# Performance work log

Measured on AMD Instinct MI355X. Metric: run time of the kernel, lower is better.

Reference implementation:

```python
import jax, jax.numpy as jnp
import numpy as np

N_NODES = 50000
N_EDGES = 1600000
IN_FEAT = 128
OUT_FEAT = 128


def setup_inputs() -> dict:
    key = jax.random.key(0)
    k_x, k_w, k_v, k_r, k_c = jax.random.split(key, 5)
    X = jax.random.normal(k_x, (N_NODES, IN_FEAT), dtype=jnp.float32)
    # nn.Linear(in_feat, out_feat, bias=False) weight: [out_feat, in_feat]
    W = jax.random.normal(k_w, (OUT_FEAT, IN_FEAT), dtype=jnp.float32) * (1.0 / np.sqrt(IN_FEAT))
    # Sparse adjacency A in COO form: A[rows[e], cols[e]] = vals[e]
    A_vals = jax.random.uniform(k_v, (N_EDGES,), dtype=jnp.float32)
    A_rows = jax.random.randint(k_r, (N_EDGES,), 0, N_NODES, dtype=jnp.int32)
    A_cols = jax.random.randint(k_c, (N_EDGES,), 0, N_NODES, dtype=jnp.int32)
    return {"X": X, "W": W, "A_vals": A_vals, "A_rows": A_rows, "A_cols": A_cols}


def reference(X, W, A_vals, A_rows, A_cols):
    # H = linear(X) = X @ W.T  -> [N, out_feat]
    H = jnp.einsum("ni,oi->no", X, W)
    # out = A @ H via COO SpMM: gather source rows, scale by edge value,
    # scatter-add into destination rows.
    msgs = A_vals[:, None] * H[A_cols]            # [E, out_feat]
    out = jax.ops.segment_sum(msgs, A_rows, num_segments=N_NODES)
    return out
```

## Files before the change

### kernel.cpp

```cpp
#include <hip/hip_runtime.h>


constexpr int N_NODES = 50000;
constexpr int N_EDGES = 1600000;
constexpr int FEAT    = 128;

constexpr int ROWS_PER_BIN = 64;
constexpr int NB           = (N_NODES + ROWS_PER_BIN - 1) / ROWS_PER_BIN;
constexpr int CAP          = 2560;
constexpr int CHUNK        = 4096;
constexpr int PART_BLOCKS  = (N_EDGES + CHUNK - 1) / CHUNK;
constexpr int GEMM_BLOCKS  = (N_NODES + 63) / 64;
constexpr int OVF_CAP      = 8192;

constexpr int SROWS = 16;
constexpr int SCAP  = 832;

__device__ __forceinline__ unsigned short f2bf(float x) {
    unsigned u = __float_as_uint(x);
    u += 0x7fffu + ((u >> 16) & 1u);
    return (unsigned short)(u >> 16);
}
__device__ __forceinline__ float bf2f(unsigned short s) {
    return __uint_as_float(((unsigned)s) << 16);
}

__global__ __launch_bounds__(256) void gemm_xwt_bf16(
    const float* __restrict__ X, const float* __restrict__ W,
    unsigned short* __restrict__ Hb, int* __restrict__ zbuf, int zn) {
    int zt = blockIdx.x * 256 + threadIdx.x;
    if (zt < zn) zbuf[zt] = 0;

    constexpr int BM = 64, BK = 32;
    __shared__ float Xs[BK][BM + 4];
    __shared__ float Ws[BK][FEAT + 4];

    const int tid = threadIdx.x;
    const int tx  = tid & 15;
    const int ty  = tid >> 4;
    const int row0 = blockIdx.x * BM;

    float acc[4][8];
#pragma unroll
    for (int i = 0; i < 4; i++)
#pragma unroll
        for (int j = 0; j < 8; j++) acc[i][j] = 0.f;

    for (int kt = 0; kt < FEAT; kt += BK) {
#pragma unroll
        for (int t = 0; t < 2; t++) {
            int idx = tid + 256 * t;
            int r   = idx >> 3;
            int kq  = (idx & 7) << 2;
            int gr  = row0 + r;
            if (gr >= N_NODES) gr = N_NODES - 1;
            const float4 v = *(const float4*)&X[gr * FEAT + kt + kq];
            Xs[kq + 0][r] = v.x; Xs[kq + 1][r] = v.y;
            Xs[kq + 2][r] = v.z; Xs[kq + 3][r] = v.w;
        }
#pragma unroll
        for (int t = 0; t < 4; t++) {
            int idx = tid + 256 * t;
            int o   = idx >> 3;
            int kq  = (idx & 7) << 2;
            const float4 v = *(const float4*)&W[o * FEAT + kt + kq];
            Ws[kq + 0][o] = v.x; Ws[kq + 1][o] = v.y;
            Ws[kq + 2][o] = v.z; Ws[kq + 3][o] = v.w;
        }
        __syncthreads();

#pragma unroll
        for (int k = 0; k < BK; k++) {
            const float4 xv = *(const float4*)&Xs[k][4 * ty];
            const float4 w0 = *(const float4*)&Ws[k][4 * tx];
            const float4 w1 = *(const float4*)&Ws[k][64 + 4 * tx];
            const float xa[4] = {xv.x, xv.y, xv.z, xv.w};
            const float wa[8] = {w0.x, w0.y, w0.z, w0.w, w1.x, w1.y, w1.z, w1.w};
#pragma unroll
            for (int i = 0; i < 4; i++)
#pragma unroll
                for (int j = 0; j < 8; j++) acc[i][j] += xa[i] * wa[j];
        }
        __syncthreads();
    }

    unsigned* Hb2 = (unsigned*)Hb;
#pragma unroll
    for (int i = 0; i < 4; i++) {
        int gr = row0 + 4 * ty + i;
        if (gr < N_NODES) {
            unsigned p0 = f2bf(acc[i][0]) | ((unsigned)f2bf(acc[i][1]) << 16);
            unsigned p1 = f2bf(acc[i][2]) | ((unsigned)f2bf(acc[i][3]) << 16);
            unsigned p2 = f2bf(acc[i][4]) | ((unsigned)f2bf(acc[i][5]) << 16);
            unsigned p3 = f2bf(acc[i][6]) | ((unsigned)f2bf(acc[i][7]) << 16);
            Hb2[gr * 64 + 2 * tx + 0]      = p0;
            Hb2[gr * 64 + 2 * tx + 1]      = p1;
            Hb2[gr * 64 + 32 + 2 * tx + 0] = p2;
            Hb2[gr * 64 + 32 + 2 * tx + 1] = p3;
        }
    }
}

__global__ __launch_bounds__(1024) void partition_edges(
    const int* __restrict__ rows, const int* __restrict__ cols,
    const float* __restrict__ vals,
    int* __restrict__ gcur, long long* __restrict__ binbuf,
    int* __restrict__ ovf_cnt, int* __restrict__ ovf) {
    __shared__ int hist[NB];
    __shared__ int wbase[NB];
    const int tid = threadIdx.x;
    const int e0  = blockIdx.x * CHUNK;

    for (int i = tid; i < NB; i += 1024) hist[i] = 0;
    __syncthreads();

    int myrow[4], myrank[4];
#pragma unroll
    for (int t = 0; t < 4; t++) {
        int e = e0 + t * 1024 + tid;
        int r = (e < N_EDGES) ? rows[e] : -1;
        myrow[t] = r;
        myrank[t] = (r >= 0) ? atomicAdd(&hist[r >> 6], 1) : 0;
    }
    __syncthreads();

    for (int i = tid; i < NB; i += 1024) {
        int c = hist[i];
        wbase[i] = (c > 0) ? atomicAdd(&gcur[i], c) : 0;
    }
    __syncthreads();

#pragma unroll
    for (int t = 0; t < 4; t++) {
        int e = e0 + t * 1024 + tid;
        int r = myrow[t];
        if (r < 0) continue;
        int b    = r >> 6;
        int rank = wbase[b] + myrank[t];
        if (rank < CAP) {
            unsigned rc  = ((unsigned)(r & 63) << 16) | (unsigned)cols[e];
            long long m = ((long long)__float_as_int(vals[e]) << 32) | (long long)rc;
            binbuf[(size_t)b * CAP + rank] = m;
        } else {
            int k = atomicAdd(ovf_cnt, 1);
            if (k < OVF_CAP) ovf[k] = e;
        }
    }
}

__global__ __launch_bounds__(256) void spmm_bins(
    const int* __restrict__ gcur, const long long* __restrict__ binbuf,
    const unsigned short* __restrict__ Hb, float* __restrict__ out) {
    __shared__ long long staged[SCAP];
    __shared__ long long sorted[SCAP];
    __shared__ int nstaged;
    __shared__ int hist[SROWS];
    __shared__ int cnt_of[SROWS];
    __shared__ int cur[SROWS];

    const int b    = blockIdx.x >> 2;
    const int sub  = blockIdx.x & 3;
    const int tid  = threadIdx.x;
    const int lane = tid & 63;
    const int w    = tid >> 6;

    if (tid == 0) nstaged = 0;
    if (tid < SROWS) { hist[tid] = 0; cur[tid] = 0; }
    __syncthreads();

    int cnt = gcur[b];
    if (cnt > CAP) cnt = CAP;
    const long long* bb = binbuf + (size_t)b * CAP;

    for (int i = tid; i < cnt; i += 256) {
        long long m = bb[i];
        int rl = (int)(((unsigned)m >> 16) & 63u);
        if ((rl >> 4) == sub) {
            int pos = atomicAdd(&nstaged, 1);
            if (pos < SCAP) {
                staged[pos] = m;
            } else {
                int col = (int)((unsigned)m & 0xffffu);
                float vv = __int_as_float((int)(m >> 32));
                int gr = b * ROWS_PER_BIN + rl;
                for (int f = 0; f < FEAT; f++)
                    atomicAdd(&out[gr * FEAT + f], vv * bf2f(Hb[col * FEAT + f]));
            }
        }
    }
    __syncthreads();
    int ns = nstaged;
    if (ns > SCAP) ns = SCAP;

    for (int i = tid; i < ns; i += 256) {
        int rl = (int)(((unsigned)staged[i] >> 16) & 15u);
        atomicAdd(&hist[rl], 1);
    }
    __syncthreads();

    if (w == 0) {
        int c = (lane < SROWS) ? hist[lane] : 0;
        if (lane < SROWS) cnt_of[lane] = c;
        int v = c;
#pragma unroll
        for (int off = 1; off < SROWS; off <<= 1) {
            int u = __shfl_up(v, off);
            if (lane >= off) v += u;
        }
        if (lane < SROWS) hist[lane] = v - c;
    }
    __syncthreads();

    for (int i = tid; i < ns; i += 256) {
        long long m = staged[i];
        int rl  = (int)(((unsigned)m >> 16) & 15u);
        int pos = hist[rl] + atomicAdd(&cur[rl], 1);
        sorted[pos] = m;
    }
    __syncthreads();

    const int row0 = b * ROWS_PER_BIN + sub * SROWS;
    const ushort2* __restrict__ Hb2 = (const ushort2*)Hb;
    float2* out2 = (float2*)out;

    for (int rr = 0; rr < 4; rr++) {
        const int rl = w * 4 + rr;
        const int gr = row0 + rl;
        if (gr >= N_NODES) break;
        const int s = hist[rl];
        const int e = s + cnt_of[rl];

        float accx = 0.f, accy = 0.f;
        int i = s;
        for (; i + 8 <= e; i += 8) {
            float v[8];
            ushort2 h[8];
#pragma unroll
            for (int j = 0; j < 8; j++) {
                long long m = sorted[i + j];
                int col = (int)((unsigned)m & 0xffffu);
                v[j] = __int_as_float((int)(m >> 32));
                h[j] = Hb2[col * 64 + lane];
            }
#pragma unroll
            for (int j = 0; j < 8; j++) {
                accx += v[j] * bf2f(h[j].x);
                accy += v[j] * bf2f(h[j].y);
            }
        }
        for (; i < e; i++) {
            long long m = sorted[i];
            int col = (int)((unsigned)m & 0xffffu);
            float vv = __int_as_float((int)(m >> 32));
            ushort2 hh = Hb2[col * 64 + lane];
            accx += vv * bf2f(hh.x);
            accy += vv * bf2f(hh.y);
        }
        out2[gr * 64 + lane] = make_float2(accx, accy);
    }
}

__global__ void fixup_ovf(const int* __restrict__ ovf_cnt, const int* __restrict__ ovf,
                          const int* __restrict__ rows, const int* __restrict__ cols,
                          const float* __restrict__ vals,
                          const unsigned short* __restrict__ Hb, float* __restrict__ out) {
    int n = *ovf_cnt;
    if (n > OVF_CAP) n = OVF_CAP;
    for (int k = blockIdx.x; k < n; k += gridDim.x) {
        int e = ovf[k];
        int r = rows[e], c = cols[e];
        float v = vals[e];
        for (int f = threadIdx.x; f < FEAT; f += blockDim.x)
            atomicAdd(&out[r * FEAT + f], v * bf2f(Hb[c * FEAT + f]));
    }
}

__global__ __launch_bounds__(256) void spmm_push_atomic(
    const int* __restrict__ rows, const int* __restrict__ cols,
    const float* __restrict__ vals, const unsigned short* __restrict__ Hb,
    float* __restrict__ out) {
    const int e    = blockIdx.x * 4 + (threadIdx.x >> 6);
    const int lane = threadIdx.x & 63;
    if (e >= N_EDGES) return;
    int r = rows[e], c = cols[e];
    float v = vals[e];
    atomicAdd(&out[r * FEAT + lane],      v * bf2f(Hb[c * FEAT + lane]));
    atomicAdd(&out[r * FEAT + 64 + lane], v * bf2f(Hb[c * FEAT + 64 + lane]));
}

extern "C" void kernel_launch(void* const* d_in, const int* in_sizes, int n_in,
                              void* d_out, int out_size, void* d_ws, size_t ws_size,
                              hipStream_t stream) {
    const float* X      = (const float*)d_in[0];
    const float* W      = (const float*)d_in[1];
    const float* A_vals = (const float*)d_in[2];
    const int*   A_rows = (const int*)d_in[3];
    const int*   A_cols = (const int*)d_in[4];
    float* out = (float*)d_out;

    auto align256 = [](size_t x) { return (x + 255) & ~size_t(255); };
    char* ws = (char*)d_ws;

    size_t off = 0;
    size_t hb_off   = off; off += align256(size_t(N_NODES) * FEAT * 2);
    size_t gcur_off = off; off += align256(size_t(NB) * sizeof(int));
    size_t ovfc_off = off; off += 256;
    size_t ovf_off  = off; off += align256(size_t(OVF_CAP) * sizeof(int));
    size_t bin_off  = off; off += size_t(NB) * CAP * sizeof(long long);
    const size_t need = off;

    unsigned short* Hb = (unsigned short*)(ws + hb_off);

    if (ws_size >= need) {
        int*       gcur    = (int*)(ws + gcur_off);
        int*       ovf_cnt = (int*)(ws + ovfc_off);
        int*       ovf     = (int*)(ws + ovf_off);
        long long* binbuf  = (long long*)(ws + bin_off);

        int zn = (int)((ovfc_off - gcur_off) / sizeof(int)) + 1;
        gemm_xwt_bf16<<<GEMM_BLOCKS, 256, 0, stream>>>(X, W, Hb, gcur, zn);
        partition_edges<<<PART_BLOCKS, 1024, 0, stream>>>(A_rows, A_cols, A_vals,
                                                          gcur, binbuf, ovf_cnt, ovf);
        spmm_bins<<<NB * 4, 256, 0, stream>>>(gcur, binbuf, Hb, out);
        fixup_ovf<<<16, 256, 0, stream>>>(ovf_cnt, ovf, A_rows, A_cols, A_vals, Hb, out);
    } else {
        gemm_xwt_bf16<<<GEMM_BLOCKS, 256, 0, stream>>>(X, W, Hb, (int*)(ws + hb_off), 0);
        hipMemsetAsync(out, 0, size_t(N_NODES) * FEAT * sizeof(float), stream);
        spmm_push_atomic<<<(N_EDGES + 3) / 4, 256, 0, stream>>>(A_rows, A_cols, A_vals, Hb, out);
    }
}
```

Baseline: 203.4 us.

## Use bf16 MFMA for X·Wᵀ, wave-aggregate staging atomics, deepen gather unroll

The FP32 SIMT GEMM is replaced by a kernel that converts X and W tiles to bf16 in shared memory and computes them with 16x16x32 bf16 MFMA instructions. In spmm_bins, the per-edge shared atomic on the staging counter becomes one atomic per wavefront, using ballot and popcount. The gather loop is unrolled to 16 edges, with an extra 4-edge tail, to keep more loads in flight. Rounding X and W to bf16 before the multiply adds precision loss, and the MFMA output stores are 2-byte scattered writes.

```diff
diff --git a/kernel.cpp b/kernel.cpp
--- a/kernel.cpp
+++ b/kernel.cpp
@@ -16,6 +16,11 @@
 constexpr int SROWS = 16;
 constexpr int SCAP  = 832;
 
+constexpr int PITCH = 136;
+
+typedef short short8 __attribute__((ext_vector_type(8)));
+typedef float f32x4  __attribute__((ext_vector_type(4)));
+
 __device__ __forceinline__ unsigned short f2bf(float x) {
     unsigned u = __float_as_uint(x);
     u += 0x7fffu + ((u >> 16) & 1u);
@@ -25,78 +30,68 @@
     return __uint_as_float(((unsigned)s) << 16);
 }
 
-__global__ __launch_bounds__(256) void gemm_xwt_bf16(
+__global__ __launch_bounds__(256) void gemm_xwt_mfma(
     const float* __restrict__ X, const float* __restrict__ W,
     unsigned short* __restrict__ Hb, int* __restrict__ zbuf, int zn) {
     int zt = blockIdx.x * 256 + threadIdx.x;
     if (zt < zn) zbuf[zt] = 0;
 
-    constexpr int BM = 64, BK = 32;
-    __shared__ float Xs[BK][BM + 4];
-    __shared__ float Ws[BK][FEAT + 4];
-
-    const int tid = threadIdx.x;
-    const int tx  = tid & 15;
-    const int ty  = tid >> 4;
-    const int row0 = blockIdx.x * BM;
-
-    float acc[4][8];
-#pragma unroll
-    for (int i = 0; i < 4; i++)
-#pragma unroll
-        for (int j = 0; j < 8; j++) acc[i][j] = 0.f;
-
-    for (int kt = 0; kt < FEAT; kt += BK) {
-#pragma unroll
-        for (int t = 0; t < 2; t++) {
-            int idx = tid + 256 * t;
-            int r   = idx >> 3;
-            int kq  = (idx & 7) << 2;
-            int gr  = row0 + r;
-            if (gr >= N_NODES) gr = N_NODES - 1;
-            const float4 v = *(const float4*)&X[gr * FEAT + kt + kq];
-            Xs[kq + 0][r] = v.x; Xs[kq + 1][r] = v.y;
-            Xs[kq + 2][r] = v.z; Xs[kq + 3][r] = v.w;
-        }
-#pragma unroll
-        for (int t = 0; t < 4; t++) {
-            int idx = tid + 256 * t;
-            int o   = idx >> 3;
-            int kq  = (idx & 7) << 2;
-            const float4 v = *(const float4*)&W[o * FEAT + kt + kq];
-            Ws[kq + 0][o] = v.x; Ws[kq + 1][o] = v.y;
-            Ws[kq + 2][o] = v.z; Ws[kq + 3][o] = v.w;
-        }
-        __syncthreads();
-
-#pragma unroll
-        for (int k = 0; k < BK; k++) {
-            const float4 xv = *(const float4*)&Xs[k][4 * ty];
-            const float4 w0 = *(const float4*)&Ws[k][4 * tx];
-            const float4 w1 = *(const float4*)&Ws[k][64 + 4 * tx];
-            const float xa[4] = {xv.x, xv.y, xv.z, xv.w};
-            const float wa[8] = {w0.x, w0.y, w0.z, w0.w, w1.x, w1.y, w1.z, w1.w};
-#pragma unroll
-            for (int i = 0; i < 4; i++)
-#pragma unroll
-                for (int j = 0; j < 8; j++) acc[i][j] += xa[i] * wa[j];
-        }
-        __syncthreads();
-    }
-
-    unsigned* Hb2 = (unsigned*)Hb;
-#pragma unroll
-    for (int i = 0; i < 4; i++) {
-        int gr = row0 + 4 * ty + i;
-        if (gr < N_NODES) {
-            unsigned p0 = f2bf(acc[i][0]) | ((unsigned)f2bf(acc[i][1]) << 16);
-            unsigned p1 = f2bf(acc[i][2]) | ((unsigned)f2bf(acc[i][3]) << 16);
-            unsigned p2 = f2bf(acc[i][4]) | ((unsigned)f2bf(acc[i][5]) << 16);
-            unsigned p3 = f2bf(acc[i][6]) | ((unsigned)f2bf(acc[i][7]) << 16);
-            Hb2[gr * 64 + 2 * tx + 0]      = p0;
-            Hb2[gr * 64 + 2 * tx + 1]      = p1;
-            Hb2[gr * 64 + 32 + 2 * tx + 0] = p2;
-            Hb2[gr * 64 + 32 + 2 * tx + 1] = p3;
+    __shared__ unsigned short Xs[64 * PITCH];
+    __shared__ unsigned short Wsh[128 * PITCH];
+
+    const int tid  = threadIdx.x;
+    const int row0 = blockIdx.x * 64;
+
+#pragma unroll
+    for (int t = 0; t < 8; t++) {
+        int idx = tid + 256 * t;
+        int r   = idx >> 5;
+        int c4  = (idx & 31) << 2;
+        int gr  = row0 + r;
+        if (gr >= N_NODES) gr = N_NODES - 1;
+        const float4 v = *(const float4*)&X[gr * FEAT + c4];
+        unsigned lo = f2bf(v.x) | ((unsigned)f2bf(v.y) << 16);
+        unsigned hi = f2bf(v.z) | ((unsigned)f2bf(v.w) << 16);
+        *(uint2*)&Xs[r * PITCH + c4] = make_uint2(lo, hi);
+    }
+#pragma unroll
+    for (int t = 0; t < 16; t++) {
+        int idx = tid + 256 * t;
+        int r   = idx >> 5;
+        int c4  = (idx & 31) << 2;
+        const float4 v = *(const float4*)&W[r * FEAT + c4];
+        unsigned lo = f2bf(v.x) | ((unsigned)f2bf(v.y) << 16);
+        unsigned hi = f2bf(v.z) | ((unsigned)f2bf(v.w) << 16);
+        *(uint2*)&Wsh[r * PITCH + c4] = make_uint2(lo, hi);
+    }
+    __syncthreads();
+
+    const int w    = tid >> 6;
+    const int lane = tid & 63;
+    const int m    = lane & 15;
+    const int q    = lane >> 4;
+
+    f32x4 acc[8];
+#pragma unroll
+    for (int t = 0; t < 8; t++) acc[t] = (f32x4){0.f, 0.f, 0.f, 0.f};
+
+#pragma unroll
+    for (int kt = 0; kt < 4; kt++) {
+        const int ko = kt * 32 + q * 8;
+        const short8 a = *(const short8*)&Xs[(16 * w + m) * PITCH + ko];
+#pragma unroll
+        for (int t = 0; t < 8; t++) {
+            const short8 b = *(const short8*)&Wsh[(16 * t + m) * PITCH + ko];
+            acc[t] = __builtin_amdgcn_mfma_f32_16x16x32_bf16(a, b, acc[t], 0, 0, 0);
+        }
+    }
+
+#pragma unroll
+    for (int t = 0; t < 8; t++) {
+#pragma unroll
+        for (int r = 0; r < 4; r++) {
+            int grow = row0 + 16 * w + q * 4 + r;
+            if (grow < N_NODES) Hb[grow * FEAT + 16 * t + m] = f2bf(acc[t][r]);
         }
     }
 }
@@ -172,14 +167,25 @@
     if (cnt > CAP) cnt = CAP;
     const long long* bb = binbuf + (size_t)b * CAP;
 
-    for (int i = tid; i < cnt; i += 256) {
-        long long m = bb[i];
-        int rl = (int)(((unsigned)m >> 16) & 63u);
-        if ((rl >> 4) == sub) {
-            int pos = atomicAdd(&nstaged, 1);
+    for (int base = 0; base < cnt; base += 256) {
+        const int i = base + tid;
+        bool pred = false;
+        long long m = 0;
+        if (i < cnt) {
+            m = bb[i];
+            pred = ((((unsigned)m >> 20) & 3u) == (unsigned)sub);
+        }
+        unsigned long long mask = __ballot(pred);
+        int nm = __popcll(mask);
+        int wb = 0;
+        if (lane == 0 && nm) wb = atomicAdd(&nstaged, nm);
+        wb = __shfl(wb, 0);
+        if (pred) {
+            int pos = wb + __popcll(mask & ((1ull << lane) - 1ull));
             if (pos < SCAP) {
                 staged[pos] = m;
             } else {
+                int rl  = (int)(((unsigned)m >> 16) & 63u);
                 int col = (int)((unsigned)m & 0xffffu);
                 float vv = __int_as_float((int)(m >> 32));
                 int gr = b * ROWS_PER_BIN + rl;
@@ -232,18 +238,34 @@
 
         float accx = 0.f, accy = 0.f;
         int i = s;
-        for (; i + 8 <= e; i += 8) {
-            float v[8];
-            ushort2 h[8];
-#pragma unroll
-            for (int j = 0; j < 8; j++) {
+        for (; i + 16 <= e; i += 16) {
+            float v[16];
+            ushort2 h[16];
+#pragma unroll
+            for (int j = 0; j < 16; j++) {
                 long long m = sorted[i + j];
                 int col = (int)((unsigned)m & 0xffffu);
                 v[j] = __int_as_float((int)(m >> 32));
                 h[j] = Hb2[col * 64 + lane];
             }
 #pragma unroll
-            for (int j = 0; j < 8; j++) {
+            for (int j = 0; j < 16; j++) {
+                accx += v[j] * bf2f(h[j].x);
+                accy += v[j] * bf2f(h[j].y);
+            }
+        }
+        for (; i + 4 <= e; i += 4) {
+            float v[4];
+            ushort2 h[4];
+#pragma unroll
+            for (int j = 0; j < 4; j++) {
+                long long m = sorted[i + j];
+                int col = (int)((unsigned)m & 0xffffu);
+                v[j] = __int_as_float((int)(m >> 32));
+                h[j] = Hb2[col * 64 + lane];
+            }
+#pragma unroll
+            for (int j = 0; j < 4; j++) {
                 accx += v[j] * bf2f(h[j].x);
                 accy += v[j] * bf2f(h[j].y);
             }
@@ -318,13 +340,13 @@
         long long* binbuf  = (long long*)(ws + bin_off);
 
         int zn = (int)((ovfc_off - gcur_off) / sizeof(int)) + 1;
-        gemm_xwt_bf16<<<GEMM_BLOCKS, 256, 0, stream>>>(X, W, Hb, gcur, zn);
+        gemm_xwt_mfma<<<GEMM_BLOCKS, 256, 0, stream>>>(X, W, Hb, gcur, zn);
         partition_edges<<<PART_BLOCKS, 1024, 0, stream>>>(A_rows, A_cols, A_vals,
                                                           gcur, binbuf, ovf_cnt, ovf);
         spmm_bins<<<NB * 4, 256, 0, stream>>>(gcur, binbuf, Hb, out);
         fixup_ovf<<<16, 256, 0, stream>>>(ovf_cnt, ovf, A_rows, A_cols, A_vals, Hb, out);
     } else {
-        gemm_xwt_bf16<<<GEMM_BLOCKS, 256, 0, stream>>>(X, W, Hb, (int*)(ws + hb_off), 0);
+        gemm_xwt_mfma<<<GEMM_BLOCKS, 256, 0, stream>>>(X, W, Hb, (int*)(ws + hb_off), 0);
         hipMemsetAsync(out, 0, size_t(N_NODES) * FEAT * sizeof(float), stream);
         spmm_push_atomic<<<(N_EDGES + 3) / 4, 256, 0, stream>>>(A_rows, A_cols, A_vals, Hb, out);
     }
```

New measurement: 186.8 us. 8.2% less time.
